# Kernel tuning notes

Hardware: AMD Instinct MI355X
Metric: run time of the kernel (lower is better)

Reference implementation:

```python
import jax, jax.numpy as jnp
import numpy as np
import math

LMAX = 2
NUM_Z = 4
N_NODES = 20000
N_GRAPHS = 5000
N_EDGES = 320000
# irreps as (mul, l, parity)
IR_SH   = [(1, 0, 1), (1, 1, -1), (1, 2, 1)]
IR_ATTR = [(NUM_Z**2, 0, 1), (NUM_Z**2, 1, -1), (NUM_Z**2, 2, 1)]
IR_MID  = [(64, 0, 1), (24, 1, 1), (24, 1, -1), (16, 2, 1), (16, 2, -1)]
IR_OUT  = [(1, 0, -1), (6, 0, 1)]


def _cg(j1, j2, j3, m1, m2, m3):
    if m1 + m2 != m3:
        return 0.0
    f = math.factorial
    pre = math.sqrt((2 * j3 + 1) * f(j3 + j1 - j2) * f(j3 - j1 + j2) * f(j1 + j2 - j3) / f(j1 + j2 + j3 + 1))
    pre *= math.sqrt(f(j3 + m3) * f(j3 - m3) * f(j1 - m1) * f(j1 + m1) * f(j2 - m2) * f(j2 + m2))
    s = 0.0
    for k in range(max(0, j2 - j3 - m1, j1 - j3 + m2), min(j1 + j2 - j3, j1 - m1, j2 + m2) + 1):
        s += (-1) ** k / (f(k) * f(j1 + j2 - j3 - k) * f(j1 - m1 - k) * f(j2 + m2 - k) * f(j3 - j2 + m1 + k) * f(j3 - j1 - m2 + k))
    return pre * s


def _u(l):
    # complex -> real spherical harmonics change of basis, m = -l..l
    U = np.zeros((2 * l + 1, 2 * l + 1), dtype=complex)
    for m in range(-l, l + 1):
        if m > 0:
            U[m + l, -m + l] = 1 / math.sqrt(2)
            U[m + l, m + l] = (-1) ** m / math.sqrt(2)
        elif m == 0:
            U[l, l] = 1.0
        else:
            U[m + l, m + l] = 1j / math.sqrt(2)
            U[m + l, -m + l] = -1j * (-1) ** (-m) / math.sqrt(2)
    return U


def _w3j(l1, l2, l3):
    C = np.zeros((2 * l1 + 1, 2 * l2 + 1, 2 * l3 + 1))
    for m1 in range(-l1, l1 + 1):
        for m2 in range(-l2, l2 + 1):
            m3 = m1 + m2
            if -l3 <= m3 <= l3:
                C[m1 + l1, m2 + l2, m3 + l3] = _cg(l1, l2, l3, m1, m2, m3)
    T = np.einsum('am,bn,co,mno->abc', _u(l1), _u(l2), _u(l3).conj(), C.astype(complex))
    T = T.real if np.abs(T.real).max() >= np.abs(T.imag).max() else T.imag
    return (T / np.linalg.norm(T)).astype(np.float32)  # Frobenius norm 1, e3nn convention


W3J = {(a, b, c): _w3j(a, b, c) for a in range(3) for b in range(3) for c in range(3) if abs(a - b) <= c <= a + b}


def _slices(ir):
    s = [0]
    for m, l, _ in ir:
        s.append(s[-1] + m * (2 * l + 1))
    return s


def _paths(ir1, ir2, iro):
    paths = []
    fan = [0] * len(iro)
    off = 0
    for a, (m1, l1, p1) in enumerate(ir1):
        for b, (m2, l2, p2) in enumerate(ir2):
            for c, (m3, l3, p3) in enumerate(iro):
                if p1 * p2 == p3 and abs(l1 - l2) <= l3 <= l1 + l2:
                    paths.append((a, b, c, off))
                    fan[c] += m1 * m2
                    off += m1 * m2 * m3
    return paths, fan, off


def _fctp(x1, x2, w, ir1, ir2, iro):
    # FullyConnectedTensorProduct: 'uvw' weighted Clebsch-Gordan contraction per path
    s1, s2 = _slices(ir1), _slices(ir2)
    paths, fan, _ = _paths(ir1, ir2, iro)
    E = x1.shape[0]
    out = [jnp.zeros((E, m * (2 * l + 1)), x1.dtype) for m, l, _ in iro]
    for a, b, c, off in paths:
        m1, l1, _ = ir1[a]
        m2, l2, _ = ir2[b]
        m3, l3, _ = iro[c]
        W = w[off:off + m1 * m2 * m3].reshape(m1, m2, m3)
        C = jnp.asarray(W3J[(l1, l2, l3)], x1.dtype)
        xa = x1[:, s1[a]:s1[a + 1]].reshape(E, m1, 2 * l1 + 1)
        xb = x2[:, s2[b]:s2[b + 1]].reshape(E, m2, 2 * l2 + 1)
        alpha = math.sqrt(2 * l3 + 1) / math.sqrt(fan[c])
        y = jnp.einsum('eui,evj,ijk,uvw->ewk', xa, xb, C, W)
        out[c] = out[c] + (alpha * y).reshape(E, -1)
    return jnp.concatenate(out, axis=1)


def _sh(v):
    # component-normalized harmonic polynomials for l=0,1,2 (normalize=False)
    x, y, z = v[:, 0], v[:, 1], v[:, 2]
    r2 = x * x + y * y + z * z
    s3, s15, s5 = math.sqrt(3.0), math.sqrt(15.0), math.sqrt(5.0)
    sh1 = s3 * jnp.stack([y, z, x], axis=1)
    sh2 = jnp.stack([s15 * x * y, s15 * y * z, 0.5 * s5 * (3 * z * z - r2), s15 * x * z, 0.5 * s15 * (x * x - y * y)], axis=1)
    return jnp.concatenate([jnp.ones_like(x)[:, None], sh1, sh2], axis=1)  # [E, 9]


def _forward(pos, w_tp1, w_tp2, z, batch, edge_src, edge_dst):
    E = edge_src.shape[0]
    ev = pos[edge_src] - pos[edge_dst]
    sh = _sh(ev)
    zz = NUM_Z * z[edge_src] + z[edge_dst]
    zzf = jax.nn.one_hot(zz, NUM_Z ** 2, dtype=sh.dtype) * NUM_Z  # [E, 16]
    # 'uvu' TensorProduct of (16x0e) with sh: outer product per l block
    blocks = [(0, 1), (1, 4), (4, 9)]
    edge_attr = jnp.concatenate([(zzf[:, :, None] * sh[:, None, a:b]).reshape(E, -1) for a, b in blocks], axis=1)
    inv_nn = 1.0 / math.sqrt(3.0)  # num_neighbors = 3
    node = jax.ops.segment_sum(sh, edge_dst, num_segments=N_NODES) * inv_nn
    ef = _fctp(node[edge_src], edge_attr, w_tp1, IR_SH, IR_ATTR, IR_MID)
    node = jax.ops.segment_sum(ef, edge_dst, num_segments=N_NODES) * inv_nn
    ef = _fctp(node[edge_src], edge_attr, w_tp2, IR_MID, IR_ATTR, IR_OUT)
    node = jax.ops.segment_sum(ef, edge_dst, num_segments=N_NODES) * inv_nn
    return jax.ops.segment_sum(node, batch, num_segments=N_GRAPHS) * 0.5  # num_nodes = 4


def setup_inputs() -> dict:
    key = jax.random.key(0)
    k = jax.random.split(key, 7)
    _, _, n1 = _paths(IR_SH, IR_ATTR, IR_MID)
    _, _, n2 = _paths(IR_MID, IR_ATTR, IR_OUT)
    return {
        'pos': jax.random.normal(k[0], (N_NODES, 3), jnp.float32),
        'z': jax.random.randint(k[1], (N_NODES,), 0, NUM_Z, jnp.int32),
        'batch': jnp.sort(jax.random.randint(k[2], (N_NODES,), 0, N_GRAPHS, jnp.int32)),
        'edge_src': jax.random.randint(k[3], (N_EDGES,), 0, N_NODES, jnp.int32),
        'edge_dst': jax.random.randint(k[4], (N_EDGES,), 0, N_NODES, jnp.int32),
        'w_tp1': jax.random.normal(k[5], (n1,), jnp.float32),
        'w_tp2': jax.random.normal(k[6], (n2,), jnp.float32),
    }


def reference(pos, z, batch, edge_src, edge_dst, w_tp1, w_tp2):
    return _forward(pos, w_tp1, w_tp2, z, batch, edge_src, edge_dst)
```

## Files before the change

### kernel.cpp

```cpp
#include <hip/hip_runtime.h>


#define N_EDGES   320000
#define NN_NODES  20000
#define NN_GRAPHS 5000

__device__ __forceinline__ void sh_from_vec(float x, float y, float z,
                                            float* B1, float* B2) {
    const float s3   = 1.7320508075688772f;
    const float s15  = 3.8729833462074170f;
    const float s5h  = 1.1180339887498949f;
    const float s15h = 1.9364916731037085f;
    B1[0] = s3 * y; B1[1] = s3 * z; B1[2] = s3 * x;
    float r2 = x * x + y * y + z * z;
    B2[0] = s15 * x * y;
    B2[1] = s15 * y * z;
    B2[2] = s5h * (3.f * z * z - r2);
    B2[3] = s15 * x * z;
    B2[4] = s15h * (x * x - y * y);
}

__global__ __launch_bounds__(256) void k_zero(const float* __restrict__ pos,
                                              int* __restrict__ counts,
                                              float* __restrict__ out,
                                              float4* __restrict__ pos4) {
    int tid = blockIdx.x * blockDim.x + threadIdx.x;
    int stride = gridDim.x * blockDim.x;
    for (int i = tid; i < NN_NODES; i += stride) counts[i] = 0;
    for (int i = tid; i < NN_GRAPHS * 7; i += stride) out[i] = 0.f;
    for (int i = tid; i < NN_NODES; i += stride) {
        float4 p;
        p.x = pos[3 * i]; p.y = pos[3 * i + 1]; p.z = pos[3 * i + 2]; p.w = 0.f;
        pos4[i] = p;
    }
}

__global__ __launch_bounds__(256) void k_hist(const int* __restrict__ edst,
                                              int* __restrict__ counts) {
    int e = blockIdx.x * blockDim.x + threadIdx.x;
    if (e < N_EDGES) atomicAdd(&counts[edst[e]], 1);
}

__global__ __launch_bounds__(1024) void k_scan(const int* __restrict__ counts,
                                               int* __restrict__ start,
                                               int* __restrict__ cursor) {
    __shared__ int sdata[1024];
    __shared__ int carry;
    int tid = threadIdx.x;
    if (tid == 0) carry = 0;
    __syncthreads();
    for (int base = 0; base < NN_NODES; base += 1024) {
        int i = base + tid;
        int v = (i < NN_NODES) ? counts[i] : 0;
        sdata[tid] = v;
        __syncthreads();
        for (int off = 1; off < 1024; off <<= 1) {
            int t = (tid >= off) ? sdata[tid - off] : 0;
            __syncthreads();
            sdata[tid] += t;
            __syncthreads();
        }
        int incl = sdata[tid];
        int c = carry;
        if (i < NN_NODES) {
            int excl = c + incl - v;
            start[i] = excl;
            cursor[i] = excl;
        }
        __syncthreads();
        if (tid == 0) carry = c + sdata[1023];
        __syncthreads();
    }
    if (tid == 0) start[NN_NODES] = carry;
}

__global__ __launch_bounds__(256) void k_fill(const int* __restrict__ esrc,
                                              const int* __restrict__ edst,
                                              const int* __restrict__ zarr,
                                              int* __restrict__ cursor,
                                              int* __restrict__ csr) {
    int e = blockIdx.x * blockDim.x + threadIdx.x;
    if (e >= N_EDGES) return;
    int d = edst[e];
    int s = esrc[e];
    int q = 4 * zarr[s] + zarr[d];
    int p = atomicAdd(&cursor[d], 1);
    csr[p] = s | (q << 16) | ((d & 15) << 20);
}

__global__ __launch_bounds__(256) void k_wprep(const float* __restrict__ w2,
                                               float* __restrict__ w2p) {
    const float cT0f =  0.02830690f;
    const float cT1f = -0.02635231f;
    const float cT2f = -0.01634300f;
    const float cT3f =  0.01265893f;
    const float cT4f =  0.02041241f;
    int idx = blockIdx.x * 256 + threadIdx.x;
    if (idx >= 16 * 64 * 64) return;
    int jj = idx & 63;
    int u  = (idx >> 6) & 63;
    int q  = idx >> 12;
    float v = 0.f;
    if (jj < 6) {
        v = cT0f * w2[(u * 16 + q) * 6 + jj];
    } else if (jj < 9) {
        if (u < 24) v = cT1f * w2[6144 + u * 16 + q];
    } else if (jj < 27) {
        int w = (jj - 9) % 6;
        if (u < 24) v = cT2f * w2[6528 + (u * 16 + q) * 6 + w];
    } else if (jj < 57) {
        int w = (jj - 27) % 6;
        if (u < 16) v = cT3f * w2[8832 + (u * 16 + q) * 6 + w];
    } else if (jj < 62) {
        if (u < 16) v = cT4f * w2[10368 + u * 16 + q];
    }
    w2p[idx] = v;
}

__global__ __launch_bounds__(256) void k_nodesh(const float4* __restrict__ pos4,
                                                const int* __restrict__ start,
                                                const int* __restrict__ csr,
                                                float* __restrict__ node_sh) {
    __shared__ float ns[16][12];
    int t = threadIdx.x;
    if (t < 192) ns[t / 12][t % 12] = 0.f;
    __syncthreads();
    int nbase = blockIdx.x * 16;
    int e0 = start[nbase], e1 = start[nbase + 16];
    for (int idx = e0 + t; idx < e1; idx += 256) {
        int pk = csr[idx];
        int s = pk & 0xFFFF;
        int r = (pk >> 20) & 15;
        float4 pd = pos4[nbase + r];
        float4 ps = pos4[s];
        float x = ps.x - pd.x;
        float y = ps.y - pd.y;
        float z = ps.z - pd.z;
        float B1[3], B2[5];
        sh_from_vec(x, y, z, B1, B2);
        float* nr = &ns[r][0];
        atomicAdd(nr + 0, 1.f);
        atomicAdd(nr + 1, B1[0]); atomicAdd(nr + 2, B1[1]); atomicAdd(nr + 3, B1[2]);
        atomicAdd(nr + 4, B2[0]); atomicAdd(nr + 5, B2[1]); atomicAdd(nr + 6, B2[2]);
        atomicAdd(nr + 7, B2[3]); atomicAdd(nr + 8, B2[4]);
    }
    __syncthreads();
    if (t < 144) {
        int r = t / 9, c = t % 9;
        const float inv_nn = 0.57735026918962576f;
        node_sh[(size_t)(nbase + r) * 12 + c] = ns[r][c] * inv_nn;
    }
}

template<int RB>
__device__ __forceinline__ void phase2_pass(const float* __restrict__ Gl,
                                            float (* __restrict__ smid)[368],
                                            const float* __restrict__ w1,
                                            int zpack, int j) {
    const int zp = zpack >> (2 * RB);
    float acc[8] = {0.f, 0.f, 0.f, 0.f, 0.f, 0.f, 0.f, 0.f};
    if (j < 64) {
        int w = j;
        for (int q = 0; q < 16; q++) {
            float wa = w1[q * 64 + w];
            float wb = w1[2048 + q * 64 + w];
            float wc = w1[5248 + q * 64 + w];
            int zdq = q & 3;
            const float* Gq = Gl + (q >> 2) * 51;
#pragma unroll
            for (int r2 = 0; r2 < 8; r2++) {
                if (((zp >> (2 * r2)) & 3) == zdq) {
                    const float* gq = Gq + (RB + r2) * 204;
                    acc[r2] += gq[0] * wa + gq[12] * wb + gq[42] * wc;
                }
            }
        }
#pragma unroll
        for (int r2 = 0; r2 < 8; r2++)
            smid[RB + r2][j] = 0.33333333333333333f * acc[r2];
    } else if (j < 136) {
        int tt = j - 64, w = tt / 3, k = tt - 3 * w;
        for (int q = 0; q < 16; q++) {
            float wa = w1[3072 + q * 24 + w];
            float wb = w1[6272 + q * 24 + w];
            int zdq = q & 3;
            const float* Gq = Gl + (q >> 2) * 51;
#pragma unroll
            for (int r2 = 0; r2 < 8; r2++) {
                if (((zp >> (2 * r2)) & 3) == zdq) {
                    const float* gq = Gq + (RB + r2) * 204;
                    acc[r2] += gq[13 + k] * wa + gq[43 + k] * wb;
                }
            }
        }
#pragma unroll
        for (int r2 = 0; r2 < 8; r2++)
            smid[RB + r2][j] = 0.70710678118654752f * acc[r2];
    } else if (j < 208) {
        int tt = j - 136, w = tt / 3, k = tt - 3 * w;
        for (int q = 0; q < 16; q++) {
            float wa = w1[1024 + q * 24 + w];
            float wb = w1[1664 + q * 24 + w];
            float wc = w1[3712 + q * 24 + w];
            float wd = w1[4608 + q * 24 + w];
            int zdq = q & 3;
            const float* Gq = Gl + (q >> 2) * 51;
#pragma unroll
            for (int r2 = 0; r2 < 8; r2++) {
                if (((zp >> (2 * r2)) & 3) == zdq) {
                    const float* gq = Gq + (RB + r2) * 204;
                    acc[r2] += gq[1 + k] * wa + gq[9 + k] * wb +
                               gq[21 + k] * wc + gq[34 + k] * wd;
                }
            }
        }
#pragma unroll
        for (int r2 = 0; r2 < 8; r2++)
            smid[RB + r2][j] = 0.5f * acc[r2];
    } else if (j < 288) {
        int tt = j - 208, w = tt / 5, k = tt - 5 * w;
        for (int q = 0; q < 16; q++) {
            float wa = w1[1408 + q * 16 + w];
            float wb = w1[3456 + q * 16 + w];
            float wc = w1[4352 + q * 16 + w];
            float wd = w1[6656 + q * 16 + w];
            int zdq = q & 3;
            const float* Gq = Gl + (q >> 2) * 51;
#pragma unroll
            for (int r2 = 0; r2 < 8; r2++) {
                if (((zp >> (2 * r2)) & 3) == zdq) {
                    const float* gq = Gq + (RB + r2) * 204;
                    acc[r2] += gq[4 + k] * wa + gq[16 + k] * wb +
                               gq[29 + k] * wc + gq[46 + k] * wd;
                }
            }
        }
#pragma unroll
        for (int r2 = 0; r2 < 8; r2++)
            smid[RB + r2][j] = 0.64549722436790280f * acc[r2];
    } else if (j < 368) {
        int tt = j - 288, w = tt / 5, k = tt - 5 * w;
        for (int q = 0; q < 16; q++) {
            float wa = w1[4096 + q * 16 + w];
            float wb = w1[4992 + q * 16 + w];
            int zdq = q & 3;
            const float* Gq = Gl + (q >> 2) * 51;
#pragma unroll
            for (int r2 = 0; r2 < 8; r2++) {
                if (((zp >> (2 * r2)) & 3) == zdq) {
                    const float* gq = Gq + (RB + r2) * 204;
                    acc[r2] += gq[24 + k] * wa + gq[37 + k] * wb;
                }
            }
        }
#pragma unroll
        for (int r2 = 0; r2 < 8; r2++)
            smid[RB + r2][j] = 0.91287092917527690f * acc[r2];
    }
}

__global__ __launch_bounds__(512, 4) void k_mid(const float4* __restrict__ pos4,
                                                const float* __restrict__ node_sh,
                                                const int* __restrict__ start,
                                                const int* __restrict__ csr,
                                                const float* __restrict__ w1,
                                                const int* __restrict__ zarr,
                                                const float* __restrict__ w2p,
                                                float* __restrict__ tab) {
    __shared__ float Gl[16 * 204];
    __shared__ float smid[16][368];
    __shared__ int szl[16];
    __shared__ int zcnt[4];
    __shared__ int zlist[4][16];
    int t = threadIdx.x;
    int nbase = blockIdx.x * 16;
    for (int i = t; i < 16 * 204; i += 512) Gl[i] = 0.f;
    if (t < 16) szl[t] = zarr[nbase + t];
    else if (t < 20) zcnt[t - 16] = 0;
    __syncthreads();

    int e0 = start[nbase], e1 = start[nbase + 16];

    const float r3  = 0.57735026918962576f;
    const float r5  = 0.44721359549995794f;
    const float r6  = 0.40824829046386302f;
    const float r10 = 0.31622776601683794f;
    const float s30 = 0.18257418583505536f;
    const float rt3 = 1.7320508075688772f;
    const float c222 = 0.58554004376911990f;
    const float q6 = 0.40824829046386302f;
    const float h6 = 0.20412414523193151f;
    const float h2 = 0.35355339059327376f;
    const float r2c = 0.70710678118654752f;

    for (int idx = e0 + t; idx < e1; idx += 512) {
        int pk = csr[idx];
        int s = pk & 0xFFFF;
        int zs = (pk >> 18) & 3;
        int r = (pk >> 20) & 15;
        float4 pd = pos4[nbase + r];
        float4 ps = pos4[s];
        float x = ps.x - pd.x;
        float y = ps.y - pd.y;
        float z = ps.z - pd.z;
        float B1[3], B2[5];
        sh_from_vec(x, y, z, B1, B2);
        const float4 nv0 = *(const float4*)(node_sh + s * 12);
        const float4 nv1 = *(const float4*)(node_sh + s * 12 + 4);
        float a0 = nv0.x;
        float A1[3] = {nv0.y, nv0.z, nv0.w};
        float A2[5] = {nv1.x, nv1.y, nv1.z, nv1.w, node_sh[s * 12 + 8]};
        float* gr = Gl + r * 204 + zs * 51;

        atomicAdd(gr + 0, a0);
        atomicAdd(gr + 1, a0 * B1[0] * r3);
        atomicAdd(gr + 2, a0 * B1[1] * r3);
        atomicAdd(gr + 3, a0 * B1[2] * r3);
        atomicAdd(gr + 4, a0 * B2[0] * r5);
        atomicAdd(gr + 5, a0 * B2[1] * r5);
        atomicAdd(gr + 6, a0 * B2[2] * r5);
        atomicAdd(gr + 7, a0 * B2[3] * r5);
        atomicAdd(gr + 8, a0 * B2[4] * r5);
        atomicAdd(gr + 9,  A1[0] * r3);
        atomicAdd(gr + 10, A1[1] * r3);
        atomicAdd(gr + 11, A1[2] * r3);
        atomicAdd(gr + 12, -r3 * (A1[0] * B1[0] + A1[1] * B1[1] + A1[2] * B1[2]));
        atomicAdd(gr + 13, -r6 * (A1[1] * B1[2] - A1[2] * B1[1]));
        atomicAdd(gr + 14, -r6 * (A1[2] * B1[0] - A1[0] * B1[2]));
        atomicAdd(gr + 15, -r6 * (A1[0] * B1[1] - A1[1] * B1[0]));
        atomicAdd(gr + 16, r10 * (A1[0] * B1[2] + A1[2] * B1[0]));
        atomicAdd(gr + 17, r10 * (A1[0] * B1[1] + A1[1] * B1[0]));
        atomicAdd(gr + 18, s30 * (2.f * A1[1] * B1[1] - A1[0] * B1[0] - A1[2] * B1[2]));
        atomicAdd(gr + 19, r10 * (A1[1] * B1[2] + A1[2] * B1[1]));
        atomicAdd(gr + 20, r10 * (A1[2] * B1[2] - A1[0] * B1[0]));
        {
            float Byy = -B2[2] * q6 - B2[4] * r2c;
            float Bzz = 2.f * B2[2] * q6;
            float Bxx = -B2[2] * q6 + B2[4] * r2c;
            float Bxy = B2[0] * r2c;
            float Byz = B2[1] * r2c;
            float Bxz = B2[3] * r2c;
            atomicAdd(gr + 21, -r5 * (Byy * A1[0] + Byz * A1[1] + Bxy * A1[2]));
            atomicAdd(gr + 22, -r5 * (Byz * A1[0] + Bzz * A1[1] + Bxz * A1[2]));
            atomicAdd(gr + 23, -r5 * (Bxy * A1[0] + Bxz * A1[1] + Bxx * A1[2]));
        }
        atomicAdd(gr + 24, -s30 * (B2[1] * A1[0] - B2[3] * A1[2] + 2.f * B2[4] * A1[1]));
        atomicAdd(gr + 25, -s30 * (-B2[0] * A1[0] - rt3 * B2[2] * A1[2] + B2[3] * A1[1] - B2[4] * A1[2]));
        atomicAdd(gr + 26, -s30 * (rt3 * B2[1] * A1[2] - rt3 * B2[3] * A1[0]));
        atomicAdd(gr + 27, -s30 * (B2[0] * A1[2] - B2[1] * A1[1] + rt3 * B2[2] * A1[0] - B2[4] * A1[0]));
        atomicAdd(gr + 28, -s30 * (-2.f * B2[0] * A1[1] + B2[1] * A1[2] + B2[3] * A1[0]));
        atomicAdd(gr + 29, A2[0] * r5);
        atomicAdd(gr + 30, A2[1] * r5);
        atomicAdd(gr + 31, A2[2] * r5);
        atomicAdd(gr + 32, A2[3] * r5);
        atomicAdd(gr + 33, A2[4] * r5);
        {
            float Ayy = -A2[2] * q6 - A2[4] * r2c;
            float Azz = 2.f * A2[2] * q6;
            float Axx = -A2[2] * q6 + A2[4] * r2c;
            float Axy = A2[0] * r2c;
            float Ayz = A2[1] * r2c;
            float Axz = A2[3] * r2c;
            atomicAdd(gr + 34, -r5 * (Ayy * B1[0] + Ayz * B1[1] + Axy * B1[2]));
            atomicAdd(gr + 35, -r5 * (Ayz * B1[0] + Azz * B1[1] + Axz * B1[2]));
            atomicAdd(gr + 36, -r5 * (Axy * B1[0] + Axz * B1[1] + Axx * B1[2]));
        }
        atomicAdd(gr + 37, s30 * (A2[1] * B1[0] - A2[3] * B1[2] + 2.f * A2[4] * B1[1]));
        atomicAdd(gr + 38, s30 * (-A2[0] * B1[0] - rt3 * A2[2] * B1[2] + A2[3] * B1[1] - A2[4] * B1[2]));
        atomicAdd(gr + 39, s30 * (rt3 * A2[1] * B1[2] - rt3 * A2[3] * B1[0]));
        atomicAdd(gr + 40, s30 * (A2[0] * B1[2] - A2[1] * B1[1] + rt3 * A2[2] * B1[0] - A2[4] * B1[0]));
        atomicAdd(gr + 41, s30 * (-2.f * A2[0] * B1[1] + A2[1] * B1[2] + A2[3] * B1[0]));
        atomicAdd(gr + 42, r5 * (A2[0] * B2[0] + A2[1] * B2[1] + A2[2] * B2[2] +
                                 A2[3] * B2[3] + A2[4] * B2[4]));
        atomicAdd(gr + 43, s30 * (-A2[0] * B2[1] + A2[1] * B2[0] +
                                  rt3 * (A2[2] * B2[3] - A2[3] * B2[2]) +
                                  A2[3] * B2[4] - A2[4] * B2[3]));
        atomicAdd(gr + 44, s30 * (-2.f * A2[0] * B2[4] + 2.f * A2[4] * B2[0] -
                                  A2[1] * B2[3] + A2[3] * B2[1]));
        atomicAdd(gr + 45, s30 * (A2[0] * B2[3] - A2[3] * B2[0] +
                                  rt3 * (A2[1] * B2[2] - A2[2] * B2[1]) +
                                  A2[1] * B2[4] - A2[4] * B2[1]));
        atomicAdd(gr + 46, -c222 * (-q6 * (A2[0] * B2[2] + A2[2] * B2[0]) +
                                    h2 * (A2[1] * B2[3] + A2[3] * B2[1])));
        atomicAdd(gr + 47, -c222 * (h6 * (A2[1] * B2[2] + A2[2] * B2[1]) -
                                    h2 * (A2[1] * B2[4] + A2[4] * B2[1]) +
                                    h2 * (A2[0] * B2[3] + A2[3] * B2[0])));
        atomicAdd(gr + 48, -c222 * (q6 * (A2[2] * B2[2] - A2[0] * B2[0] - A2[4] * B2[4]) +
                                    h6 * (A2[1] * B2[1] + A2[3] * B2[3])));
        atomicAdd(gr + 49, -c222 * (h6 * (A2[3] * B2[2] + A2[2] * B2[3]) +
                                    h2 * (A2[3] * B2[4] + A2[4] * B2[3]) +
                                    h2 * (A2[0] * B2[1] + A2[1] * B2[0])));
        atomicAdd(gr + 50, -c222 * (-q6 * (A2[4] * B2[2] + A2[2] * B2[4]) +
                                    h2 * (A2[3] * B2[3] - A2[1] * B2[1])));
    }
    __syncthreads();

    int zpack = 0;
#pragma unroll
    for (int r2 = 0; r2 < 16; r2++)
        zpack |= __builtin_amdgcn_readfirstlane(szl[r2]) << (2 * r2);

    if (t < 16) {
        int zsv = (zpack >> (2 * t)) & 3;
        int p = atomicAdd(&zcnt[zsv], 1);
        zlist[zsv][p] = t;
    }

    phase2_pass<0>(Gl, smid, w1, zpack, t);
    phase2_pass<8>(Gl, smid, w1, zpack, t);
    __syncthreads();

    {
        int wave = t >> 6;
        int lane = t & 63;
        int mbase, mstride, ulim;
        if (lane < 6)       { mbase = 0;                mstride = 1; ulim = 64; }
        else if (lane < 9)  { mbase = 64 + (lane - 6);  mstride = 3; ulim = 24; }
        else if (lane < 27) { mbase = 136 + (lane - 9) / 6;  mstride = 3; ulim = 24; }
        else if (lane < 57) { mbase = 208 + (lane - 27) / 6; mstride = 5; ulim = 16; }
        else if (lane < 62) { mbase = 288 + (lane - 57);     mstride = 5; ulim = 16; }
        else                { mbase = 0;                mstride = 0; ulim = 1; }
        int ulim1 = ulim - 1;

        int c0 = zcnt[0], c1 = zcnt[1], c2 = zcnt[2], c3 = zcnt[3];
        int np0 = (c0 + 1) >> 1, np1 = (c1 + 1) >> 1;
        int np2 = (c2 + 1) >> 1, np3 = (c3 + 1) >> 1;
        int o1 = np0, o2 = o1 + np1, o3 = o2 + np2;
        int total = o3 + np3;

        for (int item = wave; item < total; item += 8) {
            int zsv, pi, cnt;
            if (item < o1)      { zsv = 0; pi = item;      cnt = c0; }
            else if (item < o2) { zsv = 1; pi = item - o1; cnt = c1; }
            else if (item < o3) { zsv = 2; pi = item - o2; cnt = c2; }
            else                { zsv = 3; pi = item - o3; cnt = c3; }
            int r0 = zlist[zsv][2 * pi];
            int i1 = 2 * pi + 1;
            int has2 = (i1 < cnt);
            int r1 = has2 ? zlist[zsv][i1] : r0;
            const float* mr0 = &smid[r0][0];
            const float* mr1 = &smid[r1][0];
            const float* wp = w2p + (size_t)(4 * zsv) * 4096 + lane;
            float a00 = 0.f, a01 = 0.f, a02 = 0.f, a03 = 0.f;
            float a10 = 0.f, a11 = 0.f, a12 = 0.f, a13 = 0.f;
#pragma unroll 4
            for (int u = 0; u < 64; u++) {
                int um = (u < ulim) ? u : ulim1;
                float w0 = wp[u * 64];
                float w1v = wp[4096 + u * 64];
                float w2v = wp[8192 + u * 64];
                float w3v = wp[12288 + u * 64];
                float m0 = mr0[mbase + mstride * um];
                float m1 = mr1[mbase + mstride * um];
                a00 += m0 * w0;  a01 += m0 * w1v;
                a02 += m0 * w2v; a03 += m0 * w3v;
                a10 += m1 * w0;  a11 += m1 * w1v;
                a12 += m1 * w2v; a13 += m1 * w3v;
            }
            size_t b0 = ((size_t)(nbase + r0) * 4) * 64 + lane;
            tab[b0] = a00; tab[b0 + 64] = a01;
            tab[b0 + 128] = a02; tab[b0 + 192] = a03;
            if (has2) {
                size_t b1 = ((size_t)(nbase + r1) * 4) * 64 + lane;
                tab[b1] = a10; tab[b1 + 64] = a11;
                tab[b1 + 128] = a12; tab[b1 + 192] = a13;
            }
        }
    }
}

__global__ __launch_bounds__(512, 8) void k_out(const float4* __restrict__ pos4,
                                                const int* __restrict__ zarr,
                                                const int* __restrict__ batch,
                                                const int* __restrict__ start,
                                                const int* __restrict__ csr,
                                                const float* __restrict__ tab,
                                                float* __restrict__ out) {
    int wave = threadIdx.x >> 6;
    int lane = threadIdx.x & 63;
    int n = blockIdx.x * 8 + wave;
    float4 pd = pos4[n];
    int zd = zarr[n];
    int s0 = start[n], s1 = start[n + 1];

    int fsel, oidx;
    if (lane < 6)       { fsel = 0;                  oidx = lane + 1; }
    else if (lane < 9)  { fsel = 1 + (lane - 6);     oidx = 0; }
    else if (lane < 27) { fsel = 1 + (lane - 9) / 6; oidx = (lane - 9) % 6 + 1; }
    else if (lane < 57) { fsel = 4 + (lane - 27) / 6; oidx = (lane - 27) % 6 + 1; }
    else if (lane < 62) { fsel = 4 + (lane - 57);    oidx = 0; }
    else                { fsel = -1;                 oidx = 7; }
    float f0 = (fsel == 0) ? 1.f : 0.f;
    float f1 = (fsel == 1) ? 1.f : 0.f;
    float f2 = (fsel == 2) ? 1.f : 0.f;
    float f3 = (fsel == 3) ? 1.f : 0.f;
    float f4 = (fsel == 4) ? 1.f : 0.f;
    float f5 = (fsel == 5) ? 1.f : 0.f;
    float f6 = (fsel == 6) ? 1.f : 0.f;
    float f7 = (fsel == 7) ? 1.f : 0.f;
    float f8 = (fsel == 8) ? 1.f : 0.f;

    float acc = 0.f;
    for (int idx = s0; idx < s1; ++idx) {
        int pk = csr[idx];
        pk = __builtin_amdgcn_readfirstlane(pk);
        int s = pk & 0xFFFF;
        float T = tab[((size_t)s * 4 + zd) * 64 + lane];
        float4 ps = pos4[s];
        float x = ps.x - pd.x;
        float y = ps.y - pd.y;
        float z = ps.z - pd.z;
        float B1[3], B2[5];
        sh_from_vec(x, y, z, B1, B2);
        float factor = f0 + f1 * B1[0] + f2 * B1[1] + f3 * B1[2]
                     + f4 * B2[0] + f5 * B2[1] + f6 * B2[2]
                     + f7 * B2[3] + f8 * B2[4];
        acc += T * factor;
    }

    float ov[7];
#pragma unroll
    for (int w = 0; w < 7; w++) ov[w] = (oidx == w) ? acc : 0.f;
#pragma unroll
    for (int off = 32; off > 0; off >>= 1)
#pragma unroll
        for (int w = 0; w < 7; w++) ov[w] += __shfl_down(ov[w], off, 64);
    if (lane == 0) {
        float* og = out + batch[n] * 7;
#pragma unroll
        for (int w = 0; w < 7; w++) atomicAdd(og + w, ov[w]);
    }
}

extern "C" void kernel_launch(void* const* d_in, const int* in_sizes, int n_in,
                              void* d_out, int out_size, void* d_ws, size_t ws_size,
                              hipStream_t stream) {
    const float* pos  = (const float*)d_in[0];
    const int*   z    = (const int*)d_in[1];
    const int*   bat  = (const int*)d_in[2];
    const int*   esrc = (const int*)d_in[3];
    const int*   edst = (const int*)d_in[4];
    const float* w1   = (const float*)d_in[5];
    const float* w2   = (const float*)d_in[6];
    float* out = (float*)d_out;

    int*   wsI = (int*)d_ws;
    float* wsF = (float*)d_ws;
    int* counts  = wsI + 0;
    int* start   = wsI + 32768;
    int* cursor  = wsI + 65536;
    int* csr     = wsI + 98304;
    float4* pos4   = (float4*)(wsF + 425984);
    float* node_sh = wsF + 524288;
    float* w2p     = wsF + 786432;
    float* tab     = wsF + 1048576;

    k_zero<<<64, 256, 0, stream>>>(pos, counts, out, pos4);
    k_hist<<<(N_EDGES + 255) / 256, 256, 0, stream>>>(edst, counts);
    k_scan<<<1, 1024, 0, stream>>>(counts, start, cursor);
    k_fill<<<(N_EDGES + 255) / 256, 256, 0, stream>>>(esrc, edst, z, cursor, csr);
    k_wprep<<<256, 256, 0, stream>>>(w2, w2p);
    k_nodesh<<<NN_NODES / 16, 256, 0, stream>>>(pos4, start, csr, node_sh);
    k_mid<<<NN_NODES / 16, 512, 0, stream>>>(pos4, node_sh, start, csr, w1, z, w2p, tab);
    k_out<<<NN_NODES / 8, 512, 0, stream>>>(pos4, z, bat, start, csr, tab, out);
}
```

Measured before the change: 378.4 us.

## Fuse weight prep into zero kernel, wave-shuffle scan, unroll output edge loop

Folds the w2 weight-permutation kernel into the initial zeroing kernel, which drops one launch, and doubles that kernel's grid. Replaces the shared-memory Hillis-Steele scan, which needed two barriers per step, with a two-level wave-shuffle scan. Unrolls the per-edge loop in the output kernel by two so two neighbour gathers are in flight at once. The gains come from launch overhead, barriers and memory latency, at the cost of some extra registers in k_out.

After: 354.3 us. 6.4% less time.

```diff
diff --git a/kernel.cpp b/kernel.cpp
--- a/kernel.cpp
+++ b/kernel.cpp
@@ -21,9 +21,11 @@
 }
 
 __global__ __launch_bounds__(256) void k_zero(const float* __restrict__ pos,
+                                              const float* __restrict__ w2,
                                               int* __restrict__ counts,
                                               float* __restrict__ out,
-                                              float4* __restrict__ pos4) {
+                                              float4* __restrict__ pos4,
+                                              float* __restrict__ w2p) {
     int tid = blockIdx.x * blockDim.x + threadIdx.x;
     int stride = gridDim.x * blockDim.x;
     for (int i = tid; i < NN_NODES; i += stride) counts[i] = 0;
@@ -33,6 +35,31 @@
         p.x = pos[3 * i]; p.y = pos[3 * i + 1]; p.z = pos[3 * i + 2]; p.w = 0.f;
         pos4[i] = p;
     }
+    const float cT0f =  0.02830690f;
+    const float cT1f = -0.02635231f;
+    const float cT2f = -0.01634300f;
+    const float cT3f =  0.01265893f;
+    const float cT4f =  0.02041241f;
+    for (int idx = tid; idx < 16 * 64 * 64; idx += stride) {
+        int jj = idx & 63;
+        int u  = (idx >> 6) & 63;
+        int q  = idx >> 12;
+        float v = 0.f;
+        if (jj < 6) {
+            v = cT0f * w2[(u * 16 + q) * 6 + jj];
+        } else if (jj < 9) {
+            if (u < 24) v = cT1f * w2[6144 + u * 16 + q];
+        } else if (jj < 27) {
+            int w = (jj - 9) % 6;
+            if (u < 24) v = cT2f * w2[6528 + (u * 16 + q) * 6 + w];
+        } else if (jj < 57) {
+            int w = (jj - 27) % 6;
+            if (u < 16) v = cT3f * w2[8832 + (u * 16 + q) * 6 + w];
+        } else if (jj < 62) {
+            if (u < 16) v = cT4f * w2[10368 + u * 16 + q];
+        }
+        w2p[idx] = v;
+    }
 }
 
 __global__ __launch_bounds__(256) void k_hist(const int* __restrict__ edst,
@@ -44,31 +71,44 @@
 __global__ __launch_bounds__(1024) void k_scan(const int* __restrict__ counts,
                                                int* __restrict__ start,
                                                int* __restrict__ cursor) {
-    __shared__ int sdata[1024];
+    __shared__ int wsum[16];
     __shared__ int carry;
+    __shared__ int tot;
     int tid = threadIdx.x;
+    int wave = tid >> 6;
+    int lane = tid & 63;
     if (tid == 0) carry = 0;
     __syncthreads();
     for (int base = 0; base < NN_NODES; base += 1024) {
         int i = base + tid;
         int v = (i < NN_NODES) ? counts[i] : 0;
-        sdata[tid] = v;
+        int x = v;
+#pragma unroll
+        for (int off = 1; off < 64; off <<= 1) {
+            int y = __shfl_up(x, off, 64);
+            if (lane >= off) x += y;
+        }
+        if (lane == 63) wsum[wave] = x;
         __syncthreads();
-        for (int off = 1; off < 1024; off <<= 1) {
-            int t = (tid >= off) ? sdata[tid - off] : 0;
-            __syncthreads();
-            sdata[tid] += t;
-            __syncthreads();
-        }
-        int incl = sdata[tid];
-        int c = carry;
+        if (tid < 16) {
+            int w = wsum[tid];
+            int xx = w;
+#pragma unroll
+            for (int off = 1; off < 16; off <<= 1) {
+                int y = __shfl_up(xx, off, 64);
+                if (tid >= off) xx += y;
+            }
+            wsum[tid] = xx - w;
+            if (tid == 15) tot = xx;
+        }
+        __syncthreads();
+        int excl = carry + wsum[wave] + x - v;
         if (i < NN_NODES) {
-            int excl = c + incl - v;
             start[i] = excl;
             cursor[i] = excl;
         }
         __syncthreads();
-        if (tid == 0) carry = c + sdata[1023];
+        if (tid == 0) carry += tot;
         __syncthreads();
     }
     if (tid == 0) start[NN_NODES] = carry;
@@ -86,35 +126,6 @@
     int q = 4 * zarr[s] + zarr[d];
     int p = atomicAdd(&cursor[d], 1);
     csr[p] = s | (q << 16) | ((d & 15) << 20);
-}
-
-__global__ __launch_bounds__(256) void k_wprep(const float* __restrict__ w2,
-                                               float* __restrict__ w2p) {
-    const float cT0f =  0.02830690f;
-    const float cT1f = -0.02635231f;
-    const float cT2f = -0.01634300f;
-    const float cT3f =  0.01265893f;
-    const float cT4f =  0.02041241f;
-    int idx = blockIdx.x * 256 + threadIdx.x;
-    if (idx >= 16 * 64 * 64) return;
-    int jj = idx & 63;
-    int u  = (idx >> 6) & 63;
-    int q  = idx >> 12;
-    float v = 0.f;
-    if (jj < 6) {
-        v = cT0f * w2[(u * 16 + q) * 6 + jj];
-    } else if (jj < 9) {
-        if (u < 24) v = cT1f * w2[6144 + u * 16 + q];
-    } else if (jj < 27) {
-        int w = (jj - 9) % 6;
-        if (u < 24) v = cT2f * w2[6528 + (u * 16 + q) * 6 + w];
-    } else if (jj < 57) {
-        int w = (jj - 27) % 6;
-        if (u < 16) v = cT3f * w2[8832 + (u * 16 + q) * 6 + w];
-    } else if (jj < 62) {
-        if (u < 16) v = cT4f * w2[10368 + u * 16 + q];
-    }
-    w2p[idx] = v;
 }
 
 __global__ __launch_bounds__(256) void k_nodesh(const float4* __restrict__ pos4,
@@ -501,15 +512,35 @@
     float f8 = (fsel == 8) ? 1.f : 0.f;
 
     float acc = 0.f;
-    for (int idx = s0; idx < s1; ++idx) {
-        int pk = csr[idx];
-        pk = __builtin_amdgcn_readfirstlane(pk);
+    int idx = s0;
+    for (; idx + 1 < s1; idx += 2) {
+        int pkA = __builtin_amdgcn_readfirstlane(csr[idx]);
+        int pkB = __builtin_amdgcn_readfirstlane(csr[idx + 1]);
+        int sA = pkA & 0xFFFF;
+        int sB = pkB & 0xFFFF;
+        float TA = tab[((size_t)sA * 4 + zd) * 64 + lane];
+        float TB = tab[((size_t)sB * 4 + zd) * 64 + lane];
+        float4 psA = pos4[sA];
+        float4 psB = pos4[sB];
+        float xA = psA.x - pd.x, yA = psA.y - pd.y, zA = psA.z - pd.z;
+        float xB = psB.x - pd.x, yB = psB.y - pd.y, zB = psB.z - pd.z;
+        float B1A[3], B2A[5], B1B[3], B2B[5];
+        sh_from_vec(xA, yA, zA, B1A, B2A);
+        sh_from_vec(xB, yB, zB, B1B, B2B);
+        float fA = f0 + f1 * B1A[0] + f2 * B1A[1] + f3 * B1A[2]
+                 + f4 * B2A[0] + f5 * B2A[1] + f6 * B2A[2]
+                 + f7 * B2A[3] + f8 * B2A[4];
+        float fB = f0 + f1 * B1B[0] + f2 * B1B[1] + f3 * B1B[2]
+                 + f4 * B2B[0] + f5 * B2B[1] + f6 * B2B[2]
+                 + f7 * B2B[3] + f8 * B2B[4];
+        acc += TA * fA + TB * fB;
+    }
+    if (idx < s1) {
+        int pk = __builtin_amdgcn_readfirstlane(csr[idx]);
         int s = pk & 0xFFFF;
         float T = tab[((size_t)s * 4 + zd) * 64 + lane];
         float4 ps = pos4[s];
-        float x = ps.x - pd.x;
-        float y = ps.y - pd.y;
-        float z = ps.z - pd.z;
+        float x = ps.x - pd.x, y = ps.y - pd.y, z = ps.z - pd.z;
         float B1[3], B2[5];
         sh_from_vec(x, y, z, B1, B2);
         float factor = f0 + f1 * B1[0] + f2 * B1[1] + f3 * B1[2]
@@ -555,11 +586,10 @@
     float* w2p     = wsF + 786432;
     float* tab     = wsF + 1048576;
 
-    k_zero<<<64, 256, 0, stream>>>(pos, counts, out, pos4);
+    k_zero<<<128, 256, 0, stream>>>(pos, w2, counts, out, pos4, w2p);
     k_hist<<<(N_EDGES + 255) / 256, 256, 0, stream>>>(edst, counts);
     k_scan<<<1, 1024, 0, stream>>>(counts, start, cursor);
     k_fill<<<(N_EDGES + 255) / 256, 256, 0, stream>>>(esrc, edst, z, cursor, csr);
-    k_wprep<<<256, 256, 0, stream>>>(w2, w2p);
     k_nodesh<<<NN_NODES / 16, 256, 0, stream>>>(pos4, start, csr, node_sh);
     k_mid<<<NN_NODES / 16, 512, 0, stream>>>(pos4, node_sh, start, csr, w1, z, w2p, tab);
     k_out<<<NN_NODES / 8, 512, 0, stream>>>(pos4, z, bat, start, csr, tab, out);
```
